# Optimization experiments

Measured on AMD Instinct MI355X. Metric: run time of the kernel, lower is better.

Reference implementation:

```python
import jax, jax.numpy as jnp
import numpy as np

NUM_GRAPHS = 64
NEG_SLOPE_EDGE = 0.2   # GATLayer alpha
NEG_SLOPE_READ = 0.01  # torch default leaky_relu slope in ReadoutLayer


def leaky_relu(x, slope):
    return jnp.where(x >= 0, x, slope * x)


def segment_softmax(e, seg, n):
    # numerically stable softmax of edge logits grouped by destination node
    m = jax.ops.segment_max(e, seg, num_segments=n)
    m = jnp.where(jnp.isfinite(m), m, 0.0)  # guard nodes with no in-edges
    ex = jnp.exp(e - m[seg])
    s = jax.ops.segment_sum(ex, seg, num_segments=n)
    return ex / jnp.where(s > 0, s, 1.0)[seg]


def gat_layer(h, src, dst, e_feat, W, a):
    n = h.shape[0]
    out = W.shape[1]
    z = h @ W                                      # [N, out]
    a_src, a_dst, a_e = a[:out], a[out:2 * out], a[2 * out:]
    # concat([z_src, z_dst, e_feat]) @ a  ==  z_src@a_src + z_dst@a_dst + e@a_e
    logits = leaky_relu(z[src] @ a_src + z[dst] @ a_dst + e_feat @ a_e,
                        NEG_SLOPE_EDGE)            # [E]
    alpha = segment_softmax(logits, dst, n)        # [E]
    msg = alpha[:, None] * z[src]                  # [E, out]
    return jax.ops.segment_sum(msg, dst, num_segments=n)  # [N, out]


def readout(h, gid, w_att, b_att):
    # DGL mean_nodes(g, 'z', 'att'): multiply feat by weight, then mean per graph
    att = jnp.exp(leaky_relu(h @ w_att + b_att, NEG_SLOPE_READ))  # [N]
    num = jax.ops.segment_sum(att[:, None] * h, gid, num_segments=NUM_GRAPHS)
    cnt = jax.ops.segment_sum(jnp.ones_like(att), gid, num_segments=NUM_GRAPHS)
    return num / jnp.maximum(cnt, 1.0)[:, None]    # [G, hidden]


def setup_inputs() -> dict:
    key = jax.random.key(0)
    ks = jax.random.split(key, 16)
    N, E, F_IN, H, ED, C = 50000, 800000, 128, 128, 16, 10
    sc = lambda f: np.float32(1.0 / np.sqrt(f))
    return {
        "x": jax.random.normal(ks[0], (N, F_IN), jnp.float32),
        "e_feat": jax.random.normal(ks[1], (E, ED), jnp.float32),
        "src": jax.random.randint(ks[2], (E,), 0, N, dtype=jnp.int32),
        "dst": jax.random.randint(ks[3], (E,), 0, N, dtype=jnp.int32),
        "gid": jnp.sort(jax.random.randint(ks[4], (N,), 0, NUM_GRAPHS, dtype=jnp.int32)),
        "W1": jax.random.normal(ks[5], (F_IN, H), jnp.float32) * sc(F_IN),
        "a1": jax.random.normal(ks[6], (2 * H + ED,), jnp.float32) * sc(2 * H + ED),
        "W2": jax.random.normal(ks[7], (H, H), jnp.float32) * sc(H),
        "a2": jax.random.normal(ks[8], (2 * H + ED,), jnp.float32) * sc(2 * H + ED),
        "W3": jax.random.normal(ks[9], (H, H), jnp.float32) * sc(H),
        "a3": jax.random.normal(ks[10], (2 * H + ED,), jnp.float32) * sc(2 * H + ED),
        "w_att": jax.random.normal(ks[11], (H,), jnp.float32) * sc(H),
        "b_att": jnp.zeros((), jnp.float32),
        "W_cls": jax.random.normal(ks[12], (3 * H, C), jnp.float32) * sc(3 * H),
        "b_cls": jnp.zeros((C,), jnp.float32),
    }


def reference(x, e_feat, src, dst, gid, W1, a1, W2, a2, W3, a3,
              w_att, b_att, W_cls, b_cls):
    # dropout is identity at inference (training=False)
    h1 = jax.nn.relu(gat_layer(x, src, dst, e_feat, W1, a1))
    hg1 = readout(h1, gid, w_att, b_att)
    h2 = jax.nn.relu(gat_layer(h1, src, dst, e_feat, W2, a2))
    hg2 = readout(h2, gid, w_att, b_att)
    h3 = jax.nn.relu(gat_layer(h2, src, dst, e_feat, W3, a3))
    hg3 = readout(h3, gid, w_att, b_att)
    y = jnp.concatenate([hg1, hg2, hg3], axis=1) @ W_cls + b_cls  # [G, C]
    return jax.nn.log_softmax(y, axis=1)
```

## Files before the change

### kernel.cpp

```cpp
#include <hip/hip_runtime.h>
#include <math.h>

#define HD 128
#define ED 16
#define NG 64
#define NC 10

typedef short bf16x8 __attribute__((ext_vector_type(8)));
typedef float f32x4 __attribute__((ext_vector_type(4)));

__device__ __forceinline__ unsigned short f2b(float x){
  unsigned u = __float_as_uint(x);
  unsigned r = (u + 0x7fffu + ((u >> 16) & 1u)) >> 16;
  return (unsigned short)r;
}
__device__ __forceinline__ float blo(unsigned p){ return __uint_as_float(p << 16); }
__device__ __forceinline__ float bhi(unsigned p){ return __uint_as_float(p & 0xffff0000u); }
__device__ __forceinline__ float bperm_f(int idx, float v){
  return __int_as_float(__builtin_amdgcn_ds_bpermute(idx<<2, __float_as_int(v)));
}
__device__ __forceinline__ int bperm_i(int idx, int v){
  return __builtin_amdgcn_ds_bpermute(idx<<2, v);
}

__global__ void k_hist(const int* __restrict__ dst, int* __restrict__ deg, int E){
  int e4 = (blockIdx.x*blockDim.x + threadIdx.x)*4;
  if(e4+3 < E){
    int4 d = *(const int4*)&dst[e4];
    atomicAdd(&deg[d.x], 1); atomicAdd(&deg[d.y], 1);
    atomicAdd(&deg[d.z], 1); atomicAdd(&deg[d.w], 1);
  } else {
    for(int k=0;k<4;k++) if(e4+k<E) atomicAdd(&deg[dst[e4+k]], 1);
  }
}

__global__ __launch_bounds__(64) void k_bsum(const int* __restrict__ deg, int* __restrict__ bsum, int N){
  int b = blockIdx.x, t = threadIdx.x;
  int i = b*256 + t*4;
  int s = 0;
  if(i+3 < N){ int4 v = *(const int4*)&deg[i]; s = v.x+v.y+v.z+v.w; }
  else { for(int k=0;k<4;k++) if(i+k<N) s += deg[i+k]; }
  #pragma unroll
  for(int o=32;o;o>>=1) s += __shfl_xor(s,o);
  if(t==0) bsum[b] = s;
}

__global__ __launch_bounds__(1024) void k_bscan(const int* __restrict__ bsum, int* __restrict__ bbase,
                                                int* __restrict__ offs, int N, int nb){
  __shared__ int sh[1024];
  int t = threadIdx.x;
  int v = (t < nb) ? bsum[t] : 0;
  sh[t] = v; __syncthreads();
  for(int o=1;o<1024;o<<=1){ int u = (t>=o)?sh[t-o]:0; __syncthreads(); sh[t]+=u; __syncthreads(); }
  if(t < nb) bbase[t] = sh[t] - v;
  if(t == 1023) offs[N] = sh[1023];
}

__global__ __launch_bounds__(256) void k_bprop(const int* __restrict__ deg, const int* __restrict__ bbase,
                                               int* __restrict__ offs, int* __restrict__ cursor, int N){
  __shared__ int sh[256];
  int b = blockIdx.x, t = threadIdx.x;
  int i = b*256 + t;
  int v = (i<N) ? deg[i] : 0;
  sh[t] = v; __syncthreads();
  for(int o=1;o<256;o<<=1){ int u = (t>=o)?sh[t-o]:0; __syncthreads(); sh[t]+=u; __syncthreads(); }
  if(i<N){ int o_ = bbase[b] + sh[t] - v; offs[i] = o_; cursor[i] = o_; }
}

__global__ void k_scatterq(const int* __restrict__ src, const int* __restrict__ dst,
                           const float* __restrict__ ef,
                           const float* __restrict__ a1e, const float* __restrict__ a2e,
                           const float* __restrict__ a3e,
                           int* __restrict__ cursor, uint2* __restrict__ rec, int E){
  int e = blockIdx.x*blockDim.x + threadIdx.x;
  if(e>=E) return;
  const float* f = &ef[(size_t)e*ED];
  float q1=0.f, q2=0.f, q3=0.f;
  #pragma unroll
  for(int i=0;i<ED;i++){
    float fv = f[i];
    q1 = fmaf(fv, a1e[i], q1);
    q2 = fmaf(fv, a2e[i], q2);
    q3 = fmaf(fv, a3e[i], q3);
  }
  int d = dst[e];
  int p = atomicAdd(&cursor[d], 1);
  uint2 A;
  A.x = (unsigned)f2b(q1) | ((unsigned)f2b(q2) << 16);
  A.y = (unsigned)src[e] | ((unsigned)f2b(q3) << 16);
  rec[p] = A;
}

__global__ __launch_bounds__(256) void k_setup(const float* __restrict__ x, unsigned short* __restrict__ xb,
                        const float* __restrict__ W1, const float* __restrict__ W2,
                        const float* __restrict__ W3, unsigned short* __restrict__ Wb,
                        const int* __restrict__ gid, float* __restrict__ cnt,
                        int N, int ncast){
  int b = blockIdx.x;
  if(b < ncast){
    int i = (b*256 + threadIdx.x)*8;
    if(i >= N*HD) return;
    float4 v0 = *(const float4*)&x[i];
    float4 v1 = *(const float4*)&x[i+4];
    uint4 o;
    o.x = f2b(v0.x) | ((unsigned)f2b(v0.y)<<16);
    o.y = f2b(v0.z) | ((unsigned)f2b(v0.w)<<16);
    o.z = f2b(v1.x) | ((unsigned)f2b(v1.y)<<16);
    o.w = f2b(v1.z) | ((unsigned)f2b(v1.w)<<16);
    *(uint4*)&xb[i] = o;
  } else if(b < ncast + 24){
    int idx = (b - ncast)*256 + threadIdx.x;
    if(idx >= 3*2048) return;
    int layer = idx >> 11;
    int r = idx & 2047;
    const float* W = (layer==0)?W1:((layer==1)?W2:W3);
    int lane = r & 63, tile = r >> 6;
    int kt = tile >> 3, nt = tile & 7;
    int qq = lane >> 4, cc = lane & 15;
    int kbase = kt*32 + qq*8;
    int col = nt*16 + cc;
    unsigned short tmp[8];
    #pragma unroll
    for(int j=0;j<8;j++) tmp[j] = f2b(W[(size_t)(kbase+j)*HD + col]);
    uint4 o;
    o.x = tmp[0]|((unsigned)tmp[1]<<16); o.y = tmp[2]|((unsigned)tmp[3]<<16);
    o.z = tmp[4]|((unsigned)tmp[5]<<16); o.w = tmp[6]|((unsigned)tmp[7]<<16);
    *(uint4*)&Wb[(size_t)idx*8] = o;
  } else {
    int g = threadIdx.x;
    if(g >= NG) return;
    int lo=0, hi=N;
    while(lo<hi){ int mid=(lo+hi)>>1; if(gid[mid] < g) lo=mid+1; else hi=mid; }
    int start = lo; lo = start; hi = N;
    while(lo<hi){ int mid=(lo+hi)>>1; if(gid[mid] < g+1) lo=mid+1; else hi=mid; }
    cnt[g] = (float)(lo - start);
  }
}

__global__ __launch_bounds__(256) void k_gemm_mfma(
    const unsigned short* __restrict__ Ab,
    const unsigned short* __restrict__ Wb,
    unsigned short* __restrict__ Zb,
    const float* __restrict__ avec,
    float* __restrict__ ps, float* __restrict__ pd, int M)
{
  int tid = threadIdx.x;
  int w = tid >> 6, lane = tid & 63;
  int q = lane >> 4, c = lane & 15;
  int rowbase = blockIdx.x*128 + w*32;
  f32x4 acc[2][8];
  #pragma unroll
  for(int t=0;t<2;t++)
    #pragma unroll
    for(int n=0;n<8;n++) acc[t][n] = (f32x4){0.f,0.f,0.f,0.f};

  int r0 = rowbase + c;      if(r0 > M-1) r0 = M-1;
  int r1 = rowbase + 16 + c; if(r1 > M-1) r1 = M-1;
  #pragma unroll
  for(int kt=0; kt<4; kt++){
    int ko = kt*32 + q*8;
    bf16x8 a0 = __builtin_bit_cast(bf16x8, *(const uint4*)&Ab[(size_t)r0*HD + ko]);
    bf16x8 a1 = __builtin_bit_cast(bf16x8, *(const uint4*)&Ab[(size_t)r1*HD + ko]);
    #pragma unroll
    for(int n=0;n<8;n++){
      bf16x8 b = __builtin_bit_cast(bf16x8, *(const uint4*)&Wb[(((size_t)(kt*8+n))*64 + lane)*8]);
      acc[0][n] = __builtin_amdgcn_mfma_f32_16x16x32_bf16(a0, b, acc[0][n], 0,0,0);
      acc[1][n] = __builtin_amdgcn_mfma_f32_16x16x32_bf16(a1, b, acc[1][n], 0,0,0);
    }
  }
  float asv[8], adv[8];
  #pragma unroll
  for(int n=0;n<8;n++){ asv[n] = avec[n*16+c]; adv[n] = avec[HD + n*16+c]; }
  #pragma unroll
  for(int t=0;t<2;t++){
    #pragma unroll
    for(int r=0;r<4;r++){
      int grow = rowbase + t*16 + 4*q + r;
      bool ok = grow < M;
      #pragma unroll
      for(int n=0;n<8;n++){
        if(ok) Zb[(size_t)grow*HD + n*16 + c] = f2b(acc[t][n][r]);
      }
      float pp = 0.f, dd = 0.f;
      #pragma unroll
      for(int n=0;n<8;n++){ pp = fmaf(acc[t][n][r], asv[n], pp); dd = fmaf(acc[t][n][r], adv[n], dd); }
      #pragma unroll
      for(int o=1;o<16;o<<=1){ pp += __shfl_xor(pp,o); dd += __shfl_xor(dd,o); }
      if(ok && c==0){ ps[grow] = pp; pd[grow] = dd; }
    }
  }
}

__global__ __launch_bounds__(256) void k_agg2(const uint4* __restrict__ zb4,
                                              const int* __restrict__ offs,
                                              const uint2* __restrict__ rec,
                                              const float* __restrict__ ps,
                                              const float* __restrict__ pd,
                                              int layer,
                                              unsigned* __restrict__ hbu,
                                              float* __restrict__ att,
                                              const float* __restrict__ watt,
                                              const float* __restrict__ batt, int N){
  int wid = blockIdx.x*4 + (threadIdx.x>>6);
  int lane = threadIdx.x & 63;
  if(wid >= N) return;
  int q = lane >> 4, c = lane & 15;
  int d0 = offs[wid], d1 = offs[wid+1];
  float pdv = pd[wid];
  float acc[8];
  #pragma unroll
  for(int i=0;i<8;i++) acc[i]=0.f;
  float ssum = 0.f;

  for(int t0=d0; t0<d1; t0+=64){
    int rem = d1 - t0; if(rem > 64) rem = 64;
    int j = t0 + lane;
    float w = 0.f; int u = 0;
    if(j < d1){
      uint2 R = rec[j];
      u = (int)(R.y & 0xffffu);
      unsigned qb = (layer==0) ? (R.x & 0xffffu) : (layer==1 ? (R.x >> 16) : (R.y >> 16));
      float ql = __uint_as_float(qb << 16);
      float l = ps[u] + pdv + ql;
      l = (l >= 0.f) ? l : 0.2f*l;
      w = __expf(l);
    }
    float ws = w;
    #pragma unroll
    for(int o=32;o;o>>=1) ws += __shfl_xor(ws,o);
    ssum += ws;
    for(int jb=0; jb<rem; jb+=16){
      float w0 = bperm_f(jb+q,    w);  int u0 = bperm_i(jb+q,    u);
      float w1 = bperm_f(jb+4+q,  w);  int u1 = bperm_i(jb+4+q,  u);
      float w2 = bperm_f(jb+8+q,  w);  int u2 = bperm_i(jb+8+q,  u);
      float w3 = bperm_f(jb+12+q, w);  int u3 = bperm_i(jb+12+q, u);
      uint4 P0 = zb4[(size_t)u0*16 + c];
      uint4 P1 = zb4[(size_t)u1*16 + c];
      uint4 P2 = zb4[(size_t)u2*16 + c];
      uint4 P3 = zb4[(size_t)u3*16 + c];
      acc[0] = fmaf(w0, blo(P0.x), acc[0]); acc[1] = fmaf(w0, bhi(P0.x), acc[1]);
      acc[2] = fmaf(w0, blo(P0.y), acc[2]); acc[3] = fmaf(w0, bhi(P0.y), acc[3]);
      acc[4] = fmaf(w0, blo(P0.z), acc[4]); acc[5] = fmaf(w0, bhi(P0.z), acc[5]);
      acc[6] = fmaf(w0, blo(P0.w), acc[6]); acc[7] = fmaf(w0, bhi(P0.w), acc[7]);
      acc[0] = fmaf(w1, blo(P1.x), acc[0]); acc[1] = fmaf(w1, bhi(P1.x), acc[1]);
      acc[2] = fmaf(w1, blo(P1.y), acc[2]); acc[3] = fmaf(w1, bhi(P1.y), acc[3]);
      acc[4] = fmaf(w1, blo(P1.z), acc[4]); acc[5] = fmaf(w1, bhi(P1.z), acc[5]);
      acc[6] = fmaf(w1, blo(P1.w), acc[6]); acc[7] = fmaf(w1, bhi(P1.w), acc[7]);
      acc[0] = fmaf(w2, blo(P2.x), acc[0]); acc[1] = fmaf(w2, bhi(P2.x), acc[1]);
      acc[2] = fmaf(w2, blo(P2.y), acc[2]); acc[3] = fmaf(w2, bhi(P2.y), acc[3]);
      acc[4] = fmaf(w2, blo(P2.z), acc[4]); acc[5] = fmaf(w2, bhi(P2.z), acc[5]);
      acc[6] = fmaf(w2, blo(P2.w), acc[6]); acc[7] = fmaf(w2, bhi(P2.w), acc[7]);
      acc[0] = fmaf(w3, blo(P3.x), acc[0]); acc[1] = fmaf(w3, bhi(P3.x), acc[1]);
      acc[2] = fmaf(w3, blo(P3.y), acc[2]); acc[3] = fmaf(w3, bhi(P3.y), acc[3]);
      acc[4] = fmaf(w3, blo(P3.z), acc[4]); acc[5] = fmaf(w3, bhi(P3.z), acc[5]);
      acc[6] = fmaf(w3, blo(P3.w), acc[6]); acc[7] = fmaf(w3, bhi(P3.w), acc[7]);
    }
  }
  #pragma unroll
  for(int i=0;i<8;i++){ acc[i] += __shfl_xor(acc[i],16); acc[i] += __shfl_xor(acc[i],32); }
  float inv = (d1 > d0) ? 1.0f/ssum : 0.0f;
  #pragma unroll
  for(int i=0;i<8;i++) acc[i] = fmaxf(acc[i]*inv, 0.f);
  hbu[(size_t)wid*64 + c*4 + q] = (unsigned)f2b(acc[2*q]) | ((unsigned)f2b(acc[2*q+1])<<16);
  float4 w0v = *(const float4*)&watt[c*8];
  float4 w1v = *(const float4*)&watt[c*8+4];
  float t = acc[0]*w0v.x + acc[1]*w0v.y + acc[2]*w0v.z + acc[3]*w0v.w
          + acc[4]*w1v.x + acc[5]*w1v.y + acc[6]*w1v.z + acc[7]*w1v.w;
  #pragma unroll
  for(int o=1;o<16;o<<=1) t += __shfl_xor(t,o);
  t += batt[0];
  float lr = (t >= 0.f) ? t : 0.01f*t;
  if(lane==0) att[wid] = __expf(lr);
}

#define RCH 16
__global__ __launch_bounds__(64) void k_readout(const unsigned* __restrict__ hbu,
                                                const float* __restrict__ att,
                                                const int* __restrict__ gid,
                                                float* __restrict__ hg, int N){
  int g = blockIdx.x / RCH;
  int chunk = blockIdx.x % RCH;
  int t = threadIdx.x;
  int lo=0, hi=N;
  while(lo<hi){ int mid=(lo+hi)>>1; if(gid[mid] < g) lo=mid+1; else hi=mid; }
  int start = lo; lo = start; hi = N;
  while(lo<hi){ int mid=(lo+hi)>>1; if(gid[mid] < g+1) lo=mid+1; else hi=mid; }
  int end = lo;
  int len = end - start;
  int c0 = start + (int)(((long long)len * chunk) / RCH);
  int c1 = start + (int)(((long long)len * (chunk+1)) / RCH);
  float acc0 = 0.f, acc1 = 0.f;
  for(int v=c0; v<c1; v++){
    unsigned P = hbu[(size_t)v*64 + t];
    float a = att[v];
    acc0 = fmaf(a, blo(P), acc0);
    acc1 = fmaf(a, bhi(P), acc1);
  }
  atomicAdd(&hg[g*HD + 2*t],     acc0);
  atomicAdd(&hg[g*HD + 2*t + 1], acc1);
}

__global__ __launch_bounds__(384) void k_final(const float* __restrict__ hg,
                                               const float* __restrict__ cnt,
                                               const float* __restrict__ Wc,
                                               const float* __restrict__ bc,
                                               float* __restrict__ out){
  int g = blockIdx.x;
  int t = threadIdx.x;
  __shared__ float red[6];
  __shared__ float yv[NC];
  float invc = 1.f / fmaxf(cnt[g], 1.f);
  int part = t >> 7;
  int f = t & 127;
  float v = hg[(size_t)part*NG*HD + g*HD + f] * invc;
  for(int c=0; c<NC; c++){
    float p = v * Wc[(size_t)t*NC + c];
    #pragma unroll
    for(int o=32;o;o>>=1) p += __shfl_xor(p,o);
    if((t&63)==0) red[t>>6] = p;
    __syncthreads();
    if(t==0) yv[c] = bc[c] + red[0]+red[1]+red[2]+red[3]+red[4]+red[5];
    __syncthreads();
  }
  if(t==0){
    float mx = -INFINITY;
    #pragma unroll
    for(int c=0;c<NC;c++) mx = fmaxf(mx, yv[c]);
    float s = 0.f;
    #pragma unroll
    for(int c=0;c<NC;c++) s += __expf(yv[c] - mx);
    float ls = logf(s);
    #pragma unroll
    for(int c=0;c<NC;c++) out[g*NC + c] = yv[c] - mx - ls;
  }
}

extern "C" void kernel_launch(void* const* d_in, const int* in_sizes, int n_in,
                              void* d_out, int out_size, void* d_ws, size_t ws_size,
                              hipStream_t stream) {
  const float* x     = (const float*)d_in[0];
  const float* efeat = (const float*)d_in[1];
  const int*   src   = (const int*)d_in[2];
  const int*   dst   = (const int*)d_in[3];
  const int*   gid   = (const int*)d_in[4];
  const float* W1    = (const float*)d_in[5];
  const float* a1    = (const float*)d_in[6];
  const float* W2    = (const float*)d_in[7];
  const float* a2    = (const float*)d_in[8];
  const float* W3    = (const float*)d_in[9];
  const float* a3    = (const float*)d_in[10];
  const float* watt  = (const float*)d_in[11];
  const float* batt  = (const float*)d_in[12];
  const float* Wc    = (const float*)d_in[13];
  const float* bc    = (const float*)d_in[14];
  float* out = (float*)d_out;

  int N = in_sizes[4];
  int E = in_sizes[2];

  char* p = (char*)d_ws;
  auto alloc = [&](size_t bytes)->void*{
    void* r = (void*)p;
    p += (bytes + 255) & ~(size_t)255;
    return r;
  };
  unsigned short* Xb = (unsigned short*)alloc((size_t)N*HD*2);
  unsigned short* Hb = (unsigned short*)alloc((size_t)N*HD*2);
  unsigned short* Zb = (unsigned short*)alloc((size_t)N*HD*2);
  unsigned short* Wball = (unsigned short*)alloc((size_t)3*2048*8*2);
  float* ps      = (float*)alloc((size_t)N*4);
  float* pd      = (float*)alloc((size_t)N*4);
  float* att     = (float*)alloc((size_t)N*4);
  int*   deg     = (int*)  alloc((size_t)N*4);
  int*   offs    = (int*)  alloc((size_t)(N+1)*4);
  int*   cursor  = (int*)  alloc((size_t)N*4);
  uint2* rec     = (uint2*)alloc((size_t)E*8);
  int*   bsum    = (int*)  alloc((size_t)1024*4);
  int*   bbase   = (int*)  alloc((size_t)1024*4);
  float* hg      = (float*)alloc((size_t)3*NG*HD*4);
  float* cnt     = (float*)alloc((size_t)NG*4);
  (void)ws_size; (void)n_in; (void)out_size;

  int ethreads = 256;
  int eblocks = (E + ethreads - 1) / ethreads;
  int nwblocks = (N + 3) / 4;
  int nb = (N + 255) / 256;
  int ncast = (N*16 + 255) / 256;

  hipMemsetAsync(deg, 0, (size_t)N*4, stream);
  hipMemsetAsync(hg, 0, (size_t)3*NG*HD*4, stream);
  k_hist<<<(E/4 + 255)/256, 256, 0, stream>>>(dst, deg, E);
  k_bsum<<<nb, 64, 0, stream>>>(deg, bsum, N);
  k_bscan<<<1, 1024, 0, stream>>>(bsum, bbase, offs, N, nb);
  k_bprop<<<nb, 256, 0, stream>>>(deg, bbase, offs, cursor, N);
  k_scatterq<<<eblocks, ethreads, 0, stream>>>(src, dst, efeat, a1+2*HD, a2+2*HD, a3+2*HD,
                                               cursor, rec, E);
  k_setup<<<ncast + 25, 256, 0, stream>>>(x, Xb, W1, W2, W3, Wball, gid, cnt, N, ncast);

  const float* as[3] = {a1, a2, a3};
  for(int layer=0; layer<3; layer++){
    const unsigned short* Ab = (layer==0) ? Xb : Hb;
    k_gemm_mfma<<<(N+127)/128, 256, 0, stream>>>(Ab, Wball + (size_t)layer*2048*8, Zb,
                                                 as[layer], ps, pd, N);
    k_agg2<<<nwblocks, 256, 0, stream>>>((const uint4*)Zb, offs, rec, ps, pd, layer,
                                         (unsigned*)Hb, att, watt, batt, N);
    k_readout<<<NG*RCH, 64, 0, stream>>>((const unsigned*)Hb, att, gid,
                                         hg + (size_t)layer*NG*HD, N);
  }
  k_final<<<NG, 384, 0, stream>>>(hg, cnt, Wc, bc, out);
}
```

Baseline: 451.4 us.

## Use nontemporal edge loads/stores, deepen gather batching, merge memsets

```diff
diff --git a/kernel.cpp b/kernel.cpp
--- a/kernel.cpp
+++ b/kernel.cpp
@@ -8,6 +8,8 @@
 
 typedef short bf16x8 __attribute__((ext_vector_type(8)));
 typedef float f32x4 __attribute__((ext_vector_type(4)));
+typedef float f32x4v __attribute__((ext_vector_type(4)));
+typedef unsigned long long u64;
 
 __device__ __forceinline__ unsigned short f2b(float x){
   unsigned u = __float_as_uint(x);
@@ -74,21 +76,26 @@
                            int* __restrict__ cursor, uint2* __restrict__ rec, int E){
   int e = blockIdx.x*blockDim.x + threadIdx.x;
   if(e>=E) return;
-  const float* f = &ef[(size_t)e*ED];
+  const f32x4v* f4 = (const f32x4v*)&ef[(size_t)e*ED];
+  f32x4v v0 = __builtin_nontemporal_load(f4+0);
+  f32x4v v1 = __builtin_nontemporal_load(f4+1);
+  f32x4v v2 = __builtin_nontemporal_load(f4+2);
+  f32x4v v3 = __builtin_nontemporal_load(f4+3);
+  float fv[ED] = {v0.x,v0.y,v0.z,v0.w, v1.x,v1.y,v1.z,v1.w,
+                  v2.x,v2.y,v2.z,v2.w, v3.x,v3.y,v3.z,v3.w};
   float q1=0.f, q2=0.f, q3=0.f;
   #pragma unroll
   for(int i=0;i<ED;i++){
-    float fv = f[i];
-    q1 = fmaf(fv, a1e[i], q1);
-    q2 = fmaf(fv, a2e[i], q2);
-    q3 = fmaf(fv, a3e[i], q3);
+    q1 = fmaf(fv[i], a1e[i], q1);
+    q2 = fmaf(fv[i], a2e[i], q2);
+    q3 = fmaf(fv[i], a3e[i], q3);
   }
   int d = dst[e];
   int p = atomicAdd(&cursor[d], 1);
-  uint2 A;
-  A.x = (unsigned)f2b(q1) | ((unsigned)f2b(q2) << 16);
-  A.y = (unsigned)src[e] | ((unsigned)f2b(q3) << 16);
-  rec[p] = A;
+  unsigned lo = (unsigned)f2b(q1) | ((unsigned)f2b(q2) << 16);
+  unsigned hi = (unsigned)src[e] | ((unsigned)f2b(q3) << 16);
+  u64 packed = (u64)lo | ((u64)hi << 32);
+  __builtin_nontemporal_store(packed, (u64*)&rec[p]);
 }
 
 __global__ __launch_bounds__(256) void k_setup(const float* __restrict__ x, unsigned short* __restrict__ xb,
@@ -229,31 +236,23 @@
     #pragma unroll
     for(int o=32;o;o>>=1) ws += __shfl_xor(ws,o);
     ssum += ws;
-    for(int jb=0; jb<rem; jb+=16){
-      float w0 = bperm_f(jb+q,    w);  int u0 = bperm_i(jb+q,    u);
-      float w1 = bperm_f(jb+4+q,  w);  int u1 = bperm_i(jb+4+q,  u);
-      float w2 = bperm_f(jb+8+q,  w);  int u2 = bperm_i(jb+8+q,  u);
-      float w3 = bperm_f(jb+12+q, w);  int u3 = bperm_i(jb+12+q, u);
-      uint4 P0 = zb4[(size_t)u0*16 + c];
-      uint4 P1 = zb4[(size_t)u1*16 + c];
-      uint4 P2 = zb4[(size_t)u2*16 + c];
-      uint4 P3 = zb4[(size_t)u3*16 + c];
-      acc[0] = fmaf(w0, blo(P0.x), acc[0]); acc[1] = fmaf(w0, bhi(P0.x), acc[1]);
-      acc[2] = fmaf(w0, blo(P0.y), acc[2]); acc[3] = fmaf(w0, bhi(P0.y), acc[3]);
-      acc[4] = fmaf(w0, blo(P0.z), acc[4]); acc[5] = fmaf(w0, bhi(P0.z), acc[5]);
-      acc[6] = fmaf(w0, blo(P0.w), acc[6]); acc[7] = fmaf(w0, bhi(P0.w), acc[7]);
-      acc[0] = fmaf(w1, blo(P1.x), acc[0]); acc[1] = fmaf(w1, bhi(P1.x), acc[1]);
-      acc[2] = fmaf(w1, blo(P1.y), acc[2]); acc[3] = fmaf(w1, bhi(P1.y), acc[3]);
-      acc[4] = fmaf(w1, blo(P1.z), acc[4]); acc[5] = fmaf(w1, bhi(P1.z), acc[5]);
-      acc[6] = fmaf(w1, blo(P1.w), acc[6]); acc[7] = fmaf(w1, bhi(P1.w), acc[7]);
-      acc[0] = fmaf(w2, blo(P2.x), acc[0]); acc[1] = fmaf(w2, bhi(P2.x), acc[1]);
-      acc[2] = fmaf(w2, blo(P2.y), acc[2]); acc[3] = fmaf(w2, bhi(P2.y), acc[3]);
-      acc[4] = fmaf(w2, blo(P2.z), acc[4]); acc[5] = fmaf(w2, bhi(P2.z), acc[5]);
-      acc[6] = fmaf(w2, blo(P2.w), acc[6]); acc[7] = fmaf(w2, bhi(P2.w), acc[7]);
-      acc[0] = fmaf(w3, blo(P3.x), acc[0]); acc[1] = fmaf(w3, bhi(P3.x), acc[1]);
-      acc[2] = fmaf(w3, blo(P3.y), acc[2]); acc[3] = fmaf(w3, bhi(P3.y), acc[3]);
-      acc[4] = fmaf(w3, blo(P3.z), acc[4]); acc[5] = fmaf(w3, bhi(P3.z), acc[5]);
-      acc[6] = fmaf(w3, blo(P3.w), acc[6]); acc[7] = fmaf(w3, bhi(P3.w), acc[7]);
+    for(int jb=0; jb<rem; jb+=32){
+      float wv[8]; int uv[8];
+      #pragma unroll
+      for(int k=0;k<8;k++){
+        wv[k] = bperm_f(jb + 4*k + q, w);
+        uv[k] = bperm_i(jb + 4*k + q, u);
+      }
+      uint4 P[8];
+      #pragma unroll
+      for(int k=0;k<8;k++) P[k] = zb4[(size_t)uv[k]*16 + c];
+      #pragma unroll
+      for(int k=0;k<8;k++){
+        acc[0] = fmaf(wv[k], blo(P[k].x), acc[0]); acc[1] = fmaf(wv[k], bhi(P[k].x), acc[1]);
+        acc[2] = fmaf(wv[k], blo(P[k].y), acc[2]); acc[3] = fmaf(wv[k], bhi(P[k].y), acc[3]);
+        acc[4] = fmaf(wv[k], blo(P[k].z), acc[4]); acc[5] = fmaf(wv[k], bhi(P[k].z), acc[5]);
+        acc[6] = fmaf(wv[k], blo(P[k].w), acc[6]); acc[7] = fmaf(wv[k], bhi(P[k].w), acc[7]);
+      }
     }
   }
   #pragma unroll
@@ -371,13 +370,14 @@
   float* ps      = (float*)alloc((size_t)N*4);
   float* pd      = (float*)alloc((size_t)N*4);
   float* att     = (float*)alloc((size_t)N*4);
+  size_t degpad  = ((size_t)N*4 + 255) & ~(size_t)255;
   int*   deg     = (int*)  alloc((size_t)N*4);
+  float* hg      = (float*)alloc((size_t)3*NG*HD*4);
   int*   offs    = (int*)  alloc((size_t)(N+1)*4);
   int*   cursor  = (int*)  alloc((size_t)N*4);
   uint2* rec     = (uint2*)alloc((size_t)E*8);
   int*   bsum    = (int*)  alloc((size_t)1024*4);
   int*   bbase   = (int*)  alloc((size_t)1024*4);
-  float* hg      = (float*)alloc((size_t)3*NG*HD*4);
   float* cnt     = (float*)alloc((size_t)NG*4);
   (void)ws_size; (void)n_in; (void)out_size;
 
@@ -387,8 +387,7 @@
   int nb = (N + 255) / 256;
   int ncast = (N*16 + 255) / 256;
 
-  hipMemsetAsync(deg, 0, (size_t)N*4, stream);
-  hipMemsetAsync(hg, 0, (size_t)3*NG*HD*4, stream);
+  hipMemsetAsync(deg, 0, degpad + (size_t)3*NG*HD*4, stream);
   k_hist<<<(E/4 + 255)/256, 256, 0, stream>>>(dst, deg, E);
   k_bsum<<<nb, 64, 0, stream>>>(deg, bsum, N);
   k_bscan<<<1, 1024, 0, stream>>>(bsum, bbase, offs, N, nb);
```

New measurement: 467.6 us. 3.6% more time.
